# Performance work log

Hardware: AMD Instinct MI355X
Metric: run time of the kernel (lower is better)

The kernel has to match this reference:

```python
import jax, jax.numpy as jnp
import numpy as np

E = 384          # embed_dim
NH = 12          # num_heads
HD = E // NH     # head_dim = 32
NC = 16          # num_clusters
SCALE = HD ** -0.5


def setup_inputs() -> dict:
    key = jax.random.key(0)
    ks = jax.random.split(key, 6)
    b, h, w = 8, 64, 64
    x = jax.random.normal(ks[0], (b, E, h, w), jnp.float32)
    qkv_w = jax.random.normal(ks[1], (3 * E, E), jnp.float32) * 0.02
    qkv_b = jnp.zeros((3 * E,), jnp.float32)
    lepe_w = jax.random.normal(ks[2], (E, 1, 5, 5), jnp.float32) * 0.02
    lepe_b = jnp.zeros((E,), jnp.float32)
    out_w = jax.random.normal(ks[3], (E, E), jnp.float32) * 0.02
    out_b = jnp.zeros((E,), jnp.float32)
    return dict(x=x, qkv_w=qkv_w, qkv_b=qkv_b, lepe_w=lepe_w,
                lepe_b=lepe_b, out_w=out_w, out_b=out_b)


def _gather_tokens(t, idx):
    # t: (b, n, l, d), idx: (b, n, l)
    return jnp.take_along_axis(t, idx[..., None], axis=2)


def reference(x, qkv_w, qkv_b, lepe_w, lepe_b, out_w, out_b):
    b, _, h, w = x.shape
    l = h * w
    lc = l // NC  # tokens per cluster

    # 1x1 conv qkv projection (channel order: [q heads | k heads | v heads])
    qkv = jnp.einsum('bchw,oc->bohw', x, qkv_w) + qkv_b[None, :, None, None]

    # lepe: 5x5 depthwise conv on the v channel slice
    v_img = qkv[:, 2 * E:]
    lepe = jax.lax.conv_general_dilated(
        v_img, lepe_w, (1, 1), ((2, 2), (2, 2)),
        feature_group_count=E,
        dimension_numbers=('NCHW', 'OIHW', 'NCHW')) + lepe_b[None, :, None, None]

    # 'b (m n d) h w -> m b n (h w) d'
    qkv = qkv.reshape(b, 3, NH, HD, l).transpose(1, 0, 2, 4, 3)  # (3,b,n,l,d)
    q, k, v = qkv[0], qkv[1], qkv[2]
    k = k * SCALE

    # cosine-similarity sort routing (sort_sim(k, k))
    cls = jnp.mean(k, axis=2, keepdims=True)                       # (b,n,1,d)
    cls = cls / jnp.maximum(jnp.linalg.norm(cls, axis=-1, keepdims=True), 1e-12)
    kn = k / jnp.maximum(jnp.linalg.norm(k, axis=-1, keepdims=True), 1e-12)
    cos = jnp.einsum('bnod,bnld->bnl', cls, kn)                    # (b,n,l)
    idx = jnp.argsort(cos, axis=-1)                                # (b,n,l)

    qs = _gather_tokens(q, idx).reshape(b, NH, NC, lc, HD)
    ks_ = _gather_tokens(k, idx).reshape(b, NH, NC, lc, HD)
    vs = _gather_tokens(v, idx).reshape(b, NH, NC, lc, HD)

    # blockwise (per-cluster) attention
    attn = jax.nn.softmax(jnp.einsum('bncld,bncmd->bnclm', qs, ks_), axis=-1)
    o = jnp.einsum('bnclm,bncmd->bncld', attn, vs).reshape(b, NH, l, HD)

    # restore original token order (inverse permutation)
    inv = jnp.argsort(idx, axis=-1)
    o = _gather_tokens(o, inv)

    # 'b n (h w) d -> b (n d) h w'
    o = o.transpose(0, 1, 3, 2).reshape(b, E, h, w)

    res = o + lepe
    return jnp.einsum('bchw,oc->bohw', res, out_w) + out_b[None, :, None, None]
```

## Files before the change

kernel.cpp:

```cpp
#include <hip/hip_runtime.h>
#include <math.h>

#define SCALE_F 0.17677669529663687f

using bf16x8 = __attribute__((ext_vector_type(8))) __bf16;
using f32x4  = __attribute__((ext_vector_type(4))) float;
using f32x16 = __attribute__((ext_vector_type(16))) float;
using uint2e = __attribute__((ext_vector_type(2))) unsigned int;

__device__ inline unsigned short f2bf(float x) {
    unsigned int u = __builtin_bit_cast(unsigned int, x);
    unsigned int r = (u + 0x7FFFu + ((u >> 16) & 1u)) >> 16;
    return (unsigned short)r;
}
__device__ inline float bf2f(unsigned short u) {
    unsigned int x = ((unsigned int)u) << 16;
    return __builtin_bit_cast(float, x);
}
__device__ inline unsigned int packbf(float a, float b) {
    return (unsigned int)f2bf(a) | ((unsigned int)f2bf(b) << 16);
}
__device__ inline bf16x8 ldfrag(const unsigned short* p) {
    return __builtin_bit_cast(bf16x8, *reinterpret_cast<const uint4*>(p));
}

__global__ __launch_bounds__(256)
void gemm_storeT_kernel(const float* __restrict__ A, const float* __restrict__ Bmat,
                        const float* __restrict__ bias, float* __restrict__ CT,
                        int M, int N, int K, long strideB, long strideCT, int ldct,
                        int m_a_off)
{
    const int bm = blockIdx.x, bn = blockIdx.y, bz = blockIdx.z;
    const float* Bp = Bmat + (long)bz * strideB;
    float* Cp = CT + (long)bz * strideCT;
    __shared__ float As[16][132];
    __shared__ float Bs[16][132];
    const int tid = threadIdx.x;
    const int tx = tid & 15, ty = tid >> 4;
    const int m0 = bm * 128, n0 = bn * 128;
    float acc[8][8];
    #pragma unroll
    for (int i = 0; i < 8; ++i)
        #pragma unroll
        for (int j = 0; j < 8; ++j) acc[i][j] = 0.f;

    for (int k0 = 0; k0 < K; k0 += 16) {
        #pragma unroll
        for (int it = 0; it < 2; ++it) {
            int slot = tid + it * 256;
            int r = slot >> 2, cq = slot & 3;
            float4 av = *reinterpret_cast<const float4*>(&A[(long)(m_a_off + m0 + r) * K + k0 + cq * 4]);
            As[cq * 4 + 0][r] = av.x; As[cq * 4 + 1][r] = av.y;
            As[cq * 4 + 2][r] = av.z; As[cq * 4 + 3][r] = av.w;
        }
        #pragma unroll
        for (int it = 0; it < 2; ++it) {
            int slot = tid + it * 256;
            int r = slot >> 5, cq = slot & 31;
            *reinterpret_cast<float4*>(&Bs[r][cq * 4]) =
                *reinterpret_cast<const float4*>(&Bp[(long)(k0 + r) * N + n0 + cq * 4]);
        }
        __syncthreads();
        #pragma unroll
        for (int kk = 0; kk < 16; ++kk) {
            float a[8], b[8];
            *reinterpret_cast<float4*>(&a[0]) = *reinterpret_cast<const float4*>(&As[kk][ty * 8]);
            *reinterpret_cast<float4*>(&a[4]) = *reinterpret_cast<const float4*>(&As[kk][ty * 8 + 4]);
            *reinterpret_cast<float4*>(&b[0]) = *reinterpret_cast<const float4*>(&Bs[kk][tx * 8]);
            *reinterpret_cast<float4*>(&b[4]) = *reinterpret_cast<const float4*>(&Bs[kk][tx * 8 + 4]);
            #pragma unroll
            for (int i = 0; i < 8; ++i)
                #pragma unroll
                for (int j = 0; j < 8; ++j)
                    acc[i][j] += a[i] * b[j];
        }
        __syncthreads();
    }

    float bv[8];
    #pragma unroll
    for (int i = 0; i < 8; ++i) bv[i] = bias[m_a_off + m0 + ty * 8 + i];
    #pragma unroll
    for (int j = 0; j < 8; ++j) {
        long tok = n0 + tx * 8 + j;
        float* p = Cp + tok * ldct + m0 + ty * 8;
        float4 lo = make_float4(acc[0][j] + bv[0], acc[1][j] + bv[1], acc[2][j] + bv[2], acc[3][j] + bv[3]);
        float4 hi = make_float4(acc[4][j] + bv[4], acc[5][j] + bv[5], acc[6][j] + bv[6], acc[7][j] + bv[7]);
        *reinterpret_cast<float4*>(p) = lo;
        *reinterpret_cast<float4*>(p + 4) = hi;
    }
}

template<bool SPLIT, int SM>
__global__ __launch_bounds__(256)
void mfma_nt_kernel(const unsigned short* __restrict__ Ah, const unsigned short* __restrict__ Al,
                    const unsigned short* __restrict__ Bh, const unsigned short* __restrict__ Bl,
                    const float* __restrict__ bias, void* __restrict__ Cout,
                    int K, int lda, int ldb,
                    long strideAb, long strideBb, long strideCb)
{
    extern __shared__ unsigned short smem[];
    unsigned short* As  = smem;
    unsigned short* Bs  = smem + 5120;
    unsigned short* Asl = smem + 10240;
    unsigned short* Bsl = smem + 15360;
    const int bm = blockIdx.x, bn = blockIdx.y, bz = blockIdx.z;
    const unsigned short* Ap = Ah + (long)bz * strideAb;
    const unsigned short* Bp = Bh + (long)bz * strideBb;
    const unsigned short* Alp = nullptr;
    const unsigned short* Blp = nullptr;
    if constexpr (SPLIT) {
        Alp = Al + (long)bz * strideAb;
        Blp = Bl + (long)bz * strideBb;
    }
    const int tid = threadIdx.x;
    const int lane = tid & 63, wid = tid >> 6;
    const int wr = wid >> 1, wc = wid & 1;
    const int l15 = lane & 15, l4 = lane >> 4;
    const int m0 = bm * 128, n0 = bn * 128;

    const f32x4 Z4 = {0.f, 0.f, 0.f, 0.f};
    f32x4 acc[4][4];
    #pragma unroll
    for (int i = 0; i < 4; ++i)
        #pragma unroll
        for (int j = 0; j < 4; ++j) acc[i][j] = Z4;

    for (int k0 = 0; k0 < K; k0 += 32) {
        if (k0) __syncthreads();
        #pragma unroll
        for (int it = 0; it < 2; ++it) {
            int slot = tid + it * 256;
            int r = slot >> 2, cq = slot & 3;
            *reinterpret_cast<uint4*>(&As[r * 40 + cq * 8]) =
                *reinterpret_cast<const uint4*>(&Ap[(long)(m0 + r) * lda + k0 + cq * 8]);
            *reinterpret_cast<uint4*>(&Bs[r * 40 + cq * 8]) =
                *reinterpret_cast<const uint4*>(&Bp[(long)(n0 + r) * ldb + k0 + cq * 8]);
            if constexpr (SPLIT) {
                *reinterpret_cast<uint4*>(&Asl[r * 40 + cq * 8]) =
                    *reinterpret_cast<const uint4*>(&Alp[(long)(m0 + r) * lda + k0 + cq * 8]);
                *reinterpret_cast<uint4*>(&Bsl[r * 40 + cq * 8]) =
                    *reinterpret_cast<const uint4*>(&Blp[(long)(n0 + r) * ldb + k0 + cq * 8]);
            }
        }
        __syncthreads();

        bf16x8 af[4], bg[4], afl[4], bgl[4];
        #pragma unroll
        for (int f = 0; f < 4; ++f) {
            af[f] = ldfrag(&As[(wr * 64 + f * 16 + l15) * 40 + l4 * 8]);
            bg[f] = ldfrag(&Bs[(wc * 64 + f * 16 + l15) * 40 + l4 * 8]);
        }
        if constexpr (SPLIT) {
            #pragma unroll
            for (int f = 0; f < 4; ++f) {
                afl[f] = ldfrag(&Asl[(wr * 64 + f * 16 + l15) * 40 + l4 * 8]);
                bgl[f] = ldfrag(&Bsl[(wc * 64 + f * 16 + l15) * 40 + l4 * 8]);
            }
        }
        #pragma unroll
        for (int fi = 0; fi < 4; ++fi)
            #pragma unroll
            for (int fj = 0; fj < 4; ++fj) {
                acc[fi][fj] = __builtin_amdgcn_mfma_f32_16x16x32_bf16(af[fi], bg[fj], acc[fi][fj], 0, 0, 0);
                if constexpr (SPLIT) {
                    acc[fi][fj] = __builtin_amdgcn_mfma_f32_16x16x32_bf16(af[fi], bgl[fj], acc[fi][fj], 0, 0, 0);
                    acc[fi][fj] = __builtin_amdgcn_mfma_f32_16x16x32_bf16(afl[fi], bg[fj], acc[fi][fj], 0, 0, 0);
                }
            }
    }

    if constexpr (SM == 0) {
        unsigned short* Cq = (unsigned short*)Cout + (long)bz * strideCb;
        #pragma unroll
        for (int fi = 0; fi < 4; ++fi)
            #pragma unroll
            for (int fj = 0; fj < 4; ++fj) {
                const int m = m0 + wr * 64 + fi * 16 + l4 * 4;
                const int t = n0 + wc * 64 + fj * 16 + l15;
                ushort4 h;
                h.x = f2bf(acc[fi][fj][0] + bias[m + 0]);
                h.y = f2bf(acc[fi][fj][1] + bias[m + 1]);
                h.z = f2bf(acc[fi][fj][2] + bias[m + 2]);
                h.w = f2bf(acc[fi][fj][3] + bias[m + 3]);
                *reinterpret_cast<ushort4*>(&Cq[(long)t * 768 + m]) = h;
            }
    } else {
        float* Cf = (float*)Cout + (long)bz * strideCb;
        #pragma unroll
        for (int fi = 0; fi < 4; ++fi)
            #pragma unroll
            for (int fj = 0; fj < 4; ++fj) {
                const int t = m0 + wr * 64 + fi * 16 + l4 * 4;
                const int m = n0 + wc * 64 + fj * 16 + l15;
                const float bv = bias[m];
                float4 v = make_float4(acc[fi][fj][0] + bv, acc[fi][fj][1] + bv,
                                       acc[fi][fj][2] + bv, acc[fi][fj][3] + bv);
                *reinterpret_cast<float4*>(&Cf[(long)m * 4096 + t]) = v;
            }
    }
}

__global__ __launch_bounds__(256)
void convert_w_kernel(const float* __restrict__ qkv_w, const float* __restrict__ qkv_b,
                      const float* __restrict__ out_w,
                      unsigned short* __restrict__ Wqv, float* __restrict__ qvb,
                      unsigned short* __restrict__ owh, unsigned short* __restrict__ owl)
{
    const int total = 294912 + 147456 + 768;
    for (int i = blockIdx.x * 256 + threadIdx.x; i < total; i += gridDim.x * 256) {
        if (i < 294912) {
            int m = i / 384, k = i - m * 384;
            int src = (m < 384) ? m : m + 384;
            Wqv[i] = f2bf(qkv_w[(long)src * 384 + k]);
        } else if (i < 294912 + 147456) {
            int o = i - 294912;
            float w = out_w[o];
            unsigned short h = f2bf(w);
            owh[o] = h;
            owl[o] = f2bf(w - bf2f(h));
        } else {
            int m = i - 294912 - 147456;
            qvb[m] = qkv_b[(m < 384) ? m : m + 384];
        }
    }
}

__global__ __launch_bounds__(256)
void transpose_x_kernel(const float* __restrict__ x, unsigned short* __restrict__ xbT)
{
    const int t0 = blockIdx.x * 64, c0 = blockIdx.y * 64, b = blockIdx.z;
    __shared__ float tl[64][65];
    const int tid = threadIdx.x;
    #pragma unroll
    for (int i = 0; i < 16; ++i) {
        int cr = (tid >> 6) + i * 4, tc = tid & 63;
        tl[cr][tc] = x[((long)b * 384 + c0 + cr) * 4096 + t0 + tc];
    }
    __syncthreads();
    #pragma unroll
    for (int i = 0; i < 8; ++i) {
        int tr = (tid >> 5) + i * 8, c2 = (tid & 31) * 2;
        unsigned int u = (unsigned int)f2bf(tl[c2][tr]) | ((unsigned int)f2bf(tl[c2 + 1][tr]) << 16);
        *reinterpret_cast<unsigned int*>(&xbT[((long)b * 4096 + t0 + tr) * 384 + c0 + c2]) = u;
    }
}

__global__ __launch_bounds__(256)
void lepe_kernel(const unsigned short* __restrict__ qvB, const float* __restrict__ w5,
                 const float* __restrict__ wb, unsigned short* __restrict__ lepeT)
{
    const int ch0 = blockIdx.x * 16;
    const int y0 = blockIdx.y * 8;
    const int b = blockIdx.z;
    const unsigned short* vb = qvB + (long)b * 4096 * 768 + 384 + ch0;
    unsigned short* dst = lepeT + (long)b * 4096 * 384 + ch0;
    __shared__ float tile[12 * 68 * 16];
    const int tid = threadIdx.x;

    for (int i = tid; i < 12 * 68 * 16; i += 256) {
        int pix = i >> 4, c = i & 15;
        int yy = pix / 68, xx = pix % 68;
        int gy = y0 + yy - 2, gx = xx - 2;
        float v = 0.f;
        if (gy >= 0 && gy < 64 && gx >= 0 && gx < 64)
            v = bf2f(vb[(long)(gy * 64 + gx) * 768 + c]);
        tile[i] = v;
    }
    const int c = tid & 15, xo = tid >> 4;
    float f[25];
    #pragma unroll
    for (int j = 0; j < 25; ++j) f[j] = w5[(ch0 + c) * 25 + j];
    const float bv = wb[ch0 + c];
    __syncthreads();

    #pragma unroll
    for (int yy = 0; yy < 8; ++yy) {
        #pragma unroll
        for (int xq = 0; xq < 4; ++xq) {
            int x = xq * 16 + xo;
            float acc = bv;
            #pragma unroll
            for (int dy = 0; dy < 5; ++dy)
                #pragma unroll
                for (int dx = 0; dx < 5; ++dx)
                    acc += tile[((yy + dy) * 68 + (x + dx)) * 16 + c] * f[dy * 5 + dx];
            dst[(long)((y0 + yy) * 64 + x) * 384 + c] = f2bf(acc);
        }
    }
}

__global__ __launch_bounds__(256)
void cos_kernel(const float* __restrict__ Kf32, float* __restrict__ cosv)
{
    const int bn = blockIdx.x;
    const int b = bn / 12, n = bn % 12;
    const float* kb = Kf32 + (long)b * 4096 * 384 + n * 32;
    __shared__ float part[256][33];
    __shared__ float clsn[32];
    const int tid = threadIdx.x;
    float acc[32];
    #pragma unroll
    for (int d = 0; d < 32; ++d) acc[d] = 0.f;
    for (int i = 0; i < 16; ++i) {
        long tok = tid + i * 256;
        const float* kr = kb + tok * 384;
        #pragma unroll
        for (int d = 0; d < 32; ++d) acc[d] += kr[d];
    }
    #pragma unroll
    for (int d = 0; d < 32; ++d) part[tid][d] = acc[d];
    __syncthreads();
    if (tid < 32) {
        double s = 0.0;
        for (int t = 0; t < 256; ++t) s += (double)part[t][tid];
        part[0][tid] = (float)s;
    }
    __syncthreads();
    if (tid == 0) {
        double nn = 0.0;
        for (int d = 0; d < 32; ++d) { double v = (double)part[0][d]; nn += v * v; }
        double inv = 1.0 / sqrt(nn > 1e-300 ? nn : 1e-300);
        for (int d = 0; d < 32; ++d) clsn[d] = (float)((double)part[0][d] * inv);
    }
    __syncthreads();
    for (int i = 0; i < 16; ++i) {
        long tok = tid + i * 256;
        const float* kr = kb + tok * 384;
        double dot = 0.0, nrm = 0.0;
        #pragma unroll
        for (int d = 0; d < 32; ++d) {
            float kv = kr[d];
            dot += (double)clsn[d] * (double)kv;
            nrm += (double)kv * (double)kv;
        }
        double cv = dot / sqrt(nrm > 1e-300 ? nrm : 1e-300);
        cosv[(long)bn * 4096 + tok] = (float)cv;
    }
}

__global__ __launch_bounds__(512)
void sort_kernel(const float* __restrict__ cosv, int* __restrict__ idxo)
{
    const int bn = blockIdx.x;
    __shared__ float sv[4096];
    __shared__ int si[4096];
    const int tid = threadIdx.x;
    for (int i = tid; i < 4096; i += 512) { sv[i] = cosv[(long)bn * 4096 + i]; si[i] = i; }
    __syncthreads();
    for (int size = 2; size <= 4096; size <<= 1) {
        for (int stride = size >> 1; stride >= 1; stride >>= 1) {
            for (int i = tid; i < 2048; i += 512) {
                int lo = (i << 1) - (i & (stride - 1));
                int hi = lo + stride;
                bool asc = ((lo & size) == 0);
                float av = sv[lo], bvv = sv[hi];
                int ai = si[lo], bi = si[hi];
                bool agtb = (av > bvv) || (av == bvv && ai > bi);
                if (agtb == asc) {
                    sv[lo] = bvv; sv[hi] = av;
                    si[lo] = bi; si[hi] = ai;
                }
            }
            __syncthreads();
        }
    }
    for (int i = tid; i < 4096; i += 512) idxo[(long)bn * 4096 + i] = si[i];
}

__global__ __launch_bounds__(256)
void attn_kernel(const float* __restrict__ Kf32, unsigned short* __restrict__ qvB,
                 const int* __restrict__ idxbuf, const unsigned short* __restrict__ lepeT)
{
    const int cc = blockIdx.x, n = blockIdx.y, b = blockIdx.z;
    const int* ip = idxbuf + ((long)(b * 12 + n)) * 4096 + cc * 256;

    __shared__ unsigned short KsL[256][36];
    __shared__ unsigned short VsT[32][260];
    __shared__ int tokLds[256];

    const int tid = threadIdx.x;
    const int w = tid >> 6;
    const int lane = tid & 63;
    const int lo5 = lane & 31;
    const int hi = lane >> 5;
    const int hi8 = hi * 8;

    const int tk0 = ip[tid];
    tokLds[tid] = tk0;
    const long tb = (long)b * 4096 + tk0;
    const unsigned short* qrow = qvB + tb * 768 + n * 32;
    const float* krow = Kf32 + tb * 384 + n * 32;

    unsigned int Pq[16];
    #pragma unroll
    for (int i = 0; i < 4; ++i) {
        uint4 qu = *reinterpret_cast<const uint4*>(qrow + i * 8);
        Pq[4 * i + 0] = qu.x; Pq[4 * i + 1] = qu.y;
        Pq[4 * i + 2] = qu.z; Pq[4 * i + 3] = qu.w;
    }
    #pragma unroll
    for (int dq = 0; dq < 8; ++dq) {
        float4 kv = *reinterpret_cast<const float4*>(krow + dq * 4);
        ushort4 kp;
        kp.x = f2bf(kv.x * SCALE_F); kp.y = f2bf(kv.y * SCALE_F);
        kp.z = f2bf(kv.z * SCALE_F); kp.w = f2bf(kv.w * SCALE_F);
        *reinterpret_cast<ushort4*>(&KsL[tid][dq * 4]) = kp;
    }
    {
        union { uint4 u[4]; unsigned short s[32]; } vv;
        const unsigned short* vrow = qrow + 384;
        #pragma unroll
        for (int i = 0; i < 4; ++i) vv.u[i] = *reinterpret_cast<const uint4*>(vrow + i * 8);
        #pragma unroll
        for (int j = 0; j < 32; ++j) VsT[j][tid] = vv.s[j];
    }

    bf16x8 qf00, qf01, qf10, qf11;
    {
        unsigned int w0[2][4], w1[2][4];
        #pragma unroll
        for (int ks = 0; ks < 2; ++ks)
            #pragma unroll
            for (int j = 0; j < 4; ++j) {
                uint2e r = __builtin_amdgcn_permlane32_swap(Pq[ks * 8 + j], Pq[ks * 8 + 4 + j], false, false);
                w0[ks][j] = r[0];
                w1[ks][j] = r[1];
            }
        qf00 = __builtin_bit_cast(bf16x8, make_uint4(w0[0][0], w0[0][1], w0[0][2], w0[0][3]));
        qf01 = __builtin_bit_cast(bf16x8, make_uint4(w0[1][0], w0[1][1], w0[1][2], w0[1][3]));
        qf10 = __builtin_bit_cast(bf16x8, make_uint4(w1[0][0], w1[0][1], w1[0][2], w1[0][3]));
        qf11 = __builtin_bit_cast(bf16x8, make_uint4(w1[1][0], w1[1][1], w1[1][2], w1[1][3]));
    }
    __syncthreads();

    const f32x16 Z16 = {0,0,0,0,0,0,0,0,0,0,0,0,0,0,0,0};
    f32x16 o0 = Z16, o1 = Z16;
    float lsum0 = 0.f, lsum1 = 0.f;

#define LDFRAG(ARR, ROW, OFF) ({ \
    const unsigned short* _p = &ARR[ROW][OFF]; \
    union { bf16x8 v; ushort4 h[2]; } _u; \
    _u.h[0] = *reinterpret_cast<const ushort4*>(_p); \
    _u.h[1] = *reinterpret_cast<const ushort4*>(_p + 4); \
    _u.v; })

#define EXP16(S, LS) { _Pragma("unroll") for (int r = 0; r < 16; ++r) { float _e = __expf(S[r]); S[r] = _e; LS += _e; } }

#define MKPB(S, H) ({ \
    unsigned int _x0 = packbf(S[(H) * 8 + 0], S[(H) * 8 + 1]); \
    unsigned int _x1 = packbf(S[(H) * 8 + 2], S[(H) * 8 + 3]); \
    unsigned int _x2 = packbf(S[(H) * 8 + 4], S[(H) * 8 + 5]); \
    unsigned int _x3 = packbf(S[(H) * 8 + 6], S[(H) * 8 + 7]); \
    uint2e _r02 = __builtin_amdgcn_permlane32_swap(_x0, _x2, false, false); \
    uint2e _r13 = __builtin_amdgcn_permlane32_swap(_x1, _x3, false, false); \
    __builtin_bit_cast(bf16x8, make_uint4(_r02[0], _r13[0], _r02[1], _r13[1])); })

    for (int ch = 0; ch < 4; ++ch) {
        const int rb = ch * 64;
        f32x16 s00 = Z16, s01 = Z16, s10 = Z16, s11 = Z16;
        bf16x8 ka;
        ka = LDFRAG(KsL, rb + lo5, hi8);
        s00 = __builtin_amdgcn_mfma_f32_32x32x16_bf16(ka, qf00, s00, 0, 0, 0);
        s01 = __builtin_amdgcn_mfma_f32_32x32x16_bf16(ka, qf10, s01, 0, 0, 0);
        ka = LDFRAG(KsL, rb + lo5, 16 + hi8);
        s00 = __builtin_amdgcn_mfma_f32_32x32x16_bf16(ka, qf01, s00, 0, 0, 0);
        s01 = __builtin_amdgcn_mfma_f32_32x32x16_bf16(ka, qf11, s01, 0, 0, 0);
        ka = LDFRAG(KsL, rb + 32 + lo5, hi8);
        s10 = __builtin_amdgcn_mfma_f32_32x32x16_bf16(ka, qf00, s10, 0, 0, 0);
        s11 = __builtin_amdgcn_mfma_f32_32x32x16_bf16(ka, qf10, s11, 0, 0, 0);
        ka = LDFRAG(KsL, rb + 32 + lo5, 16 + hi8);
        s10 = __builtin_amdgcn_mfma_f32_32x32x16_bf16(ka, qf01, s10, 0, 0, 0);
        s11 = __builtin_amdgcn_mfma_f32_32x32x16_bf16(ka, qf11, s11, 0, 0, 0);

        EXP16(s00, lsum0); EXP16(s01, lsum1);
        EXP16(s10, lsum0); EXP16(s11, lsum1);

        bf16x8 va, pb0, pb1;
        va = LDFRAG(VsT, lo5, rb + 0 + hi8);
        pb0 = MKPB(s00, 0); pb1 = MKPB(s01, 0);
        o0 = __builtin_amdgcn_mfma_f32_32x32x16_bf16(va, pb0, o0, 0, 0, 0);
        o1 = __builtin_amdgcn_mfma_f32_32x32x16_bf16(va, pb1, o1, 0, 0, 0);
        va = LDFRAG(VsT, lo5, rb + 16 + hi8);
        pb0 = MKPB(s00, 1); pb1 = MKPB(s01, 1);
        o0 = __builtin_amdgcn_mfma_f32_32x32x16_bf16(va, pb0, o0, 0, 0, 0);
        o1 = __builtin_amdgcn_mfma_f32_32x32x16_bf16(va, pb1, o1, 0, 0, 0);
        va = LDFRAG(VsT, lo5, rb + 32 + hi8);
        pb0 = MKPB(s10, 0); pb1 = MKPB(s11, 0);
        o0 = __builtin_amdgcn_mfma_f32_32x32x16_bf16(va, pb0, o0, 0, 0, 0);
        o1 = __builtin_amdgcn_mfma_f32_32x32x16_bf16(va, pb1, o1, 0, 0, 0);
        va = LDFRAG(VsT, lo5, rb + 48 + hi8);
        pb0 = MKPB(s10, 1); pb1 = MKPB(s11, 1);
        o0 = __builtin_amdgcn_mfma_f32_32x32x16_bf16(va, pb0, o0, 0, 0, 0);
        o1 = __builtin_amdgcn_mfma_f32_32x32x16_bf16(va, pb1, o1, 0, 0, 0);
    }

    const float lf0 = lsum0 + __shfl_xor(lsum0, 32);
    const float lf1 = lsum1 + __shfl_xor(lsum1, 32);
    const float li0 = 1.f / lf0, li1 = 1.f / lf1;

    #pragma unroll
    for (int qt = 0; qt < 2; ++qt) {
        const int qrix = w * 64 + qt * 32 + lo5;
        const int tk = tokLds[qrix];
        const long tb2 = (long)b * 4096 + tk;
        unsigned short* resrow = qvB + tb2 * 768;
        const unsigned short* lp = lepeT + tb2 * 384 + n * 32;
        const float li = qt ? li1 : li0;
        const f32x16& oo = qt ? o1 : o0;
        #pragma unroll
        for (int qd = 0; qd < 4; ++qd) {
            const int d0 = qd * 8 + hi * 4;
            ushort4 lv = *reinterpret_cast<const ushort4*>(lp + d0);
            float r0 = oo[qd * 4 + 0] * li + bf2f(lv.x);
            float r1 = oo[qd * 4 + 1] * li + bf2f(lv.y);
            float r2 = oo[qd * 4 + 2] * li + bf2f(lv.z);
            float r3 = oo[qd * 4 + 3] * li + bf2f(lv.w);
            unsigned short h0 = f2bf(r0), h1 = f2bf(r1), h2 = f2bf(r2), h3 = f2bf(r3);
            ushort4 hh = {h0, h1, h2, h3};
            ushort4 ll = {f2bf(r0 - bf2f(h0)), f2bf(r1 - bf2f(h1)),
                          f2bf(r2 - bf2f(h2)), f2bf(r3 - bf2f(h3))};
            *reinterpret_cast<ushort4*>(resrow + n * 32 + d0) = hh;
            *reinterpret_cast<ushort4*>(resrow + 384 + n * 32 + d0) = ll;
        }
    }
#undef LDFRAG
#undef EXP16
#undef MKPB
}

extern "C" void kernel_launch(void* const* d_in, const int* in_sizes, int n_in,
                              void* d_out, int out_size, void* d_ws, size_t ws_size,
                              hipStream_t stream)
{
    const float* x      = (const float*)d_in[0];
    const float* qkv_w  = (const float*)d_in[1];
    const float* qkv_b  = (const float*)d_in[2];
    const float* lepe_w = (const float*)d_in[3];
    const float* lepe_b = (const float*)d_in[4];
    const float* out_w  = (const float*)d_in[5];
    const float* out_b  = (const float*)d_in[6];
    float* out = (float*)d_out;

    char* ws = (char*)d_ws;
    float*          Kf32 = (float*)ws;
    unsigned short* qvB  = (unsigned short*)(ws + 50331648);
    float*          cosv = (float*)(ws + 100663296);
    int*            idx  = (int*)(ws + 102236160);
    unsigned short* Wqv  = (unsigned short*)(ws + 103809024);
    unsigned short* owh  = (unsigned short*)(ws + 104398848);
    unsigned short* owl  = (unsigned short*)(ws + 104693760);
    float*          qvb  = (float*)(ws + 104988672);

    unsigned short* xbT   = (unsigned short*)d_out;
    unsigned short* lepeT = (unsigned short*)d_out + 12582912;

    convert_w_kernel<<<1731, 256, 0, stream>>>(qkv_w, qkv_b, out_w, Wqv, qvb, owh, owl);
    transpose_x_kernel<<<dim3(64, 6, 8), 256, 0, stream>>>(x, xbT);
    gemm_storeT_kernel<<<dim3(3, 32, 8), 256, 0, stream>>>(qkv_w, x, qkv_b, Kf32,
                                                           1152, 4096, 384,
                                                           (long)384 * 4096, (long)4096 * 384, 384, 384);
    mfma_nt_kernel<false, 0><<<dim3(6, 32, 8), 256, 20480, stream>>>(
        Wqv, nullptr, xbT, nullptr, qvb, qvB,
        384, 384, 384, 0L, (long)4096 * 384, (long)4096 * 768);
    lepe_kernel<<<dim3(24, 8, 8), 256, 0, stream>>>(qvB, lepe_w, lepe_b, lepeT);
    cos_kernel<<<96, 256, 0, stream>>>(Kf32, cosv);
    sort_kernel<<<96, 512, 0, stream>>>(cosv, idx);
    attn_kernel<<<dim3(16, 12, 8), 256, 0, stream>>>(Kf32, qvB, idx, lepeT);
    mfma_nt_kernel<true, 1><<<dim3(32, 3, 8), 256, 40960, stream>>>(
        qvB, qvB + 384, owh, owl, out_b, out,
        384, 768, 384, (long)4096 * 768, 0L, (long)384 * 4096);
}
```

Measured before the change: 458.4 us.

## Double-buffer fp32 K-projection GEMM with register prefetch; widen bitonic sort blocks

The fp32 K-projection GEMM now double-buffers its shared-memory tiles and prefetches the next K-slice into registers while computing the current one. This removes one barrier per iteration and hides global load latency. The B tile is also stored in a permuted layout so each thread's two float4 reads fall on different banks. The bitonic sort kernel runs with 1024 threads instead of 512, giving more threads per block for the 96 small sorts, at the cost of doubled shared memory for the GEMM and higher register pressure.

```diff
diff --git a/kernel.cpp b/kernel.cpp
--- a/kernel.cpp
+++ b/kernel.cpp
@@ -33,48 +33,75 @@
     const int bm = blockIdx.x, bn = blockIdx.y, bz = blockIdx.z;
     const float* Bp = Bmat + (long)bz * strideB;
     float* Cp = CT + (long)bz * strideCT;
-    __shared__ float As[16][132];
-    __shared__ float Bs[16][132];
+    __shared__ float As[2][16][132];
+    __shared__ float BsF[2][16 * 136];
     const int tid = threadIdx.x;
     const int tx = tid & 15, ty = tid >> 4;
     const int m0 = bm * 128, n0 = bn * 128;
+
+    const int rA0 = tid >> 2,          cA0 = tid & 3;
+    const int rA1 = (tid + 256) >> 2,  cA1 = (tid + 256) & 3;
+    const int rB0 = tid >> 5,          cB0 = tid & 31;
+    const int rB1 = (tid + 256) >> 5,  cB1 = (tid + 256) & 31;
+    const int wB0 = rB0 * 136 + ((cB0 & 1) << 6) + ((cB0 >> 1) << 2);
+    const int wB1 = rB1 * 136 + ((cB1 & 1) << 6) + ((cB1 >> 1) << 2);
+
     float acc[8][8];
     #pragma unroll
     for (int i = 0; i < 8; ++i)
         #pragma unroll
         for (int j = 0; j < 8; ++j) acc[i][j] = 0.f;
 
-    for (int k0 = 0; k0 < K; k0 += 16) {
-        #pragma unroll
-        for (int it = 0; it < 2; ++it) {
-            int slot = tid + it * 256;
-            int r = slot >> 2, cq = slot & 3;
-            float4 av = *reinterpret_cast<const float4*>(&A[(long)(m_a_off + m0 + r) * K + k0 + cq * 4]);
-            As[cq * 4 + 0][r] = av.x; As[cq * 4 + 1][r] = av.y;
-            As[cq * 4 + 2][r] = av.z; As[cq * 4 + 3][r] = av.w;
-        }
-        #pragma unroll
-        for (int it = 0; it < 2; ++it) {
-            int slot = tid + it * 256;
-            int r = slot >> 5, cq = slot & 31;
-            *reinterpret_cast<float4*>(&Bs[r][cq * 4]) =
-                *reinterpret_cast<const float4*>(&Bp[(long)(k0 + r) * N + n0 + cq * 4]);
-        }
-        __syncthreads();
+    float4 aPf0, aPf1, bPf0, bPf1;
+    aPf0 = *reinterpret_cast<const float4*>(&A[(long)(m_a_off + m0 + rA0) * K + cA0 * 4]);
+    aPf1 = *reinterpret_cast<const float4*>(&A[(long)(m_a_off + m0 + rA1) * K + cA1 * 4]);
+    bPf0 = *reinterpret_cast<const float4*>(&Bp[(long)rB0 * N + n0 + cB0 * 4]);
+    bPf1 = *reinterpret_cast<const float4*>(&Bp[(long)rB1 * N + n0 + cB1 * 4]);
+    {
+        As[0][cA0 * 4 + 0][rA0] = aPf0.x; As[0][cA0 * 4 + 1][rA0] = aPf0.y;
+        As[0][cA0 * 4 + 2][rA0] = aPf0.z; As[0][cA0 * 4 + 3][rA0] = aPf0.w;
+        As[0][cA1 * 4 + 0][rA1] = aPf1.x; As[0][cA1 * 4 + 1][rA1] = aPf1.y;
+        As[0][cA1 * 4 + 2][rA1] = aPf1.z; As[0][cA1 * 4 + 3][rA1] = aPf1.w;
+        *reinterpret_cast<float4*>(&BsF[0][wB0]) = bPf0;
+        *reinterpret_cast<float4*>(&BsF[0][wB1]) = bPf1;
+    }
+    __syncthreads();
+
+    int p = 0;
+    const int NT = K / 16;
+    for (int kt = 0; kt < NT; ++kt) {
+        const bool last = (kt == NT - 1);
+        if (!last) {
+            const int kn = (kt + 1) * 16;
+            aPf0 = *reinterpret_cast<const float4*>(&A[(long)(m_a_off + m0 + rA0) * K + kn + cA0 * 4]);
+            aPf1 = *reinterpret_cast<const float4*>(&A[(long)(m_a_off + m0 + rA1) * K + kn + cA1 * 4]);
+            bPf0 = *reinterpret_cast<const float4*>(&Bp[(long)(kn + rB0) * N + n0 + cB0 * 4]);
+            bPf1 = *reinterpret_cast<const float4*>(&Bp[(long)(kn + rB1) * N + n0 + cB1 * 4]);
+        }
         #pragma unroll
         for (int kk = 0; kk < 16; ++kk) {
             float a[8], b[8];
-            *reinterpret_cast<float4*>(&a[0]) = *reinterpret_cast<const float4*>(&As[kk][ty * 8]);
-            *reinterpret_cast<float4*>(&a[4]) = *reinterpret_cast<const float4*>(&As[kk][ty * 8 + 4]);
-            *reinterpret_cast<float4*>(&b[0]) = *reinterpret_cast<const float4*>(&Bs[kk][tx * 8]);
-            *reinterpret_cast<float4*>(&b[4]) = *reinterpret_cast<const float4*>(&Bs[kk][tx * 8 + 4]);
+            *reinterpret_cast<float4*>(&a[0]) = *reinterpret_cast<const float4*>(&As[p][kk][ty * 8]);
+            *reinterpret_cast<float4*>(&a[4]) = *reinterpret_cast<const float4*>(&As[p][kk][ty * 8 + 4]);
+            *reinterpret_cast<float4*>(&b[0]) = *reinterpret_cast<const float4*>(&BsF[p][kk * 136 + tx * 4]);
+            *reinterpret_cast<float4*>(&b[4]) = *reinterpret_cast<const float4*>(&BsF[p][kk * 136 + 64 + tx * 4]);
             #pragma unroll
             for (int i = 0; i < 8; ++i)
                 #pragma unroll
                 for (int j = 0; j < 8; ++j)
                     acc[i][j] += a[i] * b[j];
         }
-        __syncthreads();
+        if (!last) {
+            const int q = p ^ 1;
+            As[q][cA0 * 4 + 0][rA0] = aPf0.x; As[q][cA0 * 4 + 1][rA0] = aPf0.y;
+            As[q][cA0 * 4 + 2][rA0] = aPf0.z; As[q][cA0 * 4 + 3][rA0] = aPf0.w;
+            As[q][cA1 * 4 + 0][rA1] = aPf1.x; As[q][cA1 * 4 + 1][rA1] = aPf1.y;
+            As[q][cA1 * 4 + 2][rA1] = aPf1.z; As[q][cA1 * 4 + 3][rA1] = aPf1.w;
+            *reinterpret_cast<float4*>(&BsF[q][wB0]) = bPf0;
+            *reinterpret_cast<float4*>(&BsF[q][wB1]) = bPf1;
+            __syncthreads();
+            p = q;
+        }
     }
 
     float bv[8];
@@ -83,11 +110,11 @@
     #pragma unroll
     for (int j = 0; j < 8; ++j) {
         long tok = n0 + tx * 8 + j;
-        float* p = Cp + tok * ldct + m0 + ty * 8;
+        float* ptr = Cp + tok * ldct + m0 + ty * 8;
         float4 lo = make_float4(acc[0][j] + bv[0], acc[1][j] + bv[1], acc[2][j] + bv[2], acc[3][j] + bv[3]);
         float4 hi = make_float4(acc[4][j] + bv[4], acc[5][j] + bv[5], acc[6][j] + bv[6], acc[7][j] + bv[7]);
-        *reinterpret_cast<float4*>(p) = lo;
-        *reinterpret_cast<float4*>(p + 4) = hi;
+        *reinterpret_cast<float4*>(ptr) = lo;
+        *reinterpret_cast<float4*>(ptr + 4) = hi;
     }
 }
 
@@ -339,18 +366,19 @@
     }
 }
 
-__global__ __launch_bounds__(512)
+__global__ __launch_bounds__(1024)
 void sort_kernel(const float* __restrict__ cosv, int* __restrict__ idxo)
 {
     const int bn = blockIdx.x;
     __shared__ float sv[4096];
     __shared__ int si[4096];
     const int tid = threadIdx.x;
-    for (int i = tid; i < 4096; i += 512) { sv[i] = cosv[(long)bn * 4096 + i]; si[i] = i; }
+    for (int i = tid; i < 4096; i += 1024) { sv[i] = cosv[(long)bn * 4096 + i]; si[i] = i; }
     __syncthreads();
     for (int size = 2; size <= 4096; size <<= 1) {
         for (int stride = size >> 1; stride >= 1; stride >>= 1) {
-            for (int i = tid; i < 2048; i += 512) {
+            #pragma unroll 2
+            for (int i = tid; i < 2048; i += 1024) {
                 int lo = (i << 1) - (i & (stride - 1));
                 int hi = lo + stride;
                 bool asc = ((lo & size) == 0);
@@ -365,7 +393,7 @@
             __syncthreads();
         }
     }
-    for (int i = tid; i < 4096; i += 512) idxo[(long)bn * 4096 + i] = si[i];
+    for (int i = tid; i < 4096; i += 1024) idxo[(long)bn * 4096 + i] = si[i];
 }
 
 __global__ __launch_bounds__(256)
@@ -565,7 +593,7 @@
         384, 384, 384, 0L, (long)4096 * 384, (long)4096 * 768);
     lepe_kernel<<<dim3(24, 8, 8), 256, 0, stream>>>(qvB, lepe_w, lepe_b, lepeT);
     cos_kernel<<<96, 256, 0, stream>>>(Kf32, cosv);
-    sort_kernel<<<96, 512, 0, stream>>>(cosv, idx);
+    sort_kernel<<<96, 1024, 0, stream>>>(cosv, idx);
     attn_kernel<<<dim3(16, 12, 8), 256, 0, stream>>>(Kf32, qvB, idx, lepeT);
     mfma_nt_kernel<true, 1><<<dim3(32, 3, 8), 256, 40960, stream>>>(
         qvB, qvB + 384, owh, owl, out_b, out,
```

Measured after the change: 507.5 us. +10.7%, slower.
